# Kernel tuning notes

Hardware: AMD Instinct MI355X
Metric: run time of the kernel (lower is better)

The kernel has to match this reference:

```python
import jax, jax.numpy as jnp
import numpy as np

D = 256; H = 8; DK = D // H
NT, NW, ND = 2000, 50000, 20000
E_TT, E_WT, E_TD, E_WD = 128000, 256000, 320000, 320000
SQRT_DK = float(np.sqrt(DK))


def setup_inputs() -> dict:
    key = jax.random.key(0)
    ks = jax.random.split(key, 32)
    def nrm(i, shape, s=0.05):
        return jax.random.normal(ks[i], shape, jnp.float32) * s
    inp = {
        "feat_topic": nrm(0, (NT, D), 1.0),
        "feat_word": nrm(1, (NW, D), 1.0),
        "feat_doc": nrm(2, (ND, D), 1.0),
        "ht_prev": nrm(3, (NT, D), 1.0),
        # stacked per-ntype linears, index: 0=topic, 1=word, 2=doc
        "Wk": nrm(4, (3, D, D)), "bk": nrm(5, (3, D)),
        "Wq": nrm(6, (3, D, D)), "bq": nrm(7, (3, D)),
        "Wv": nrm(8, (3, D, D)), "bv": nrm(9, (3, D)),
        # a_linears, index: 0=topic, 1=doc
        "Wa": nrm(10, (2, D, D)), "ba": nrm(11, (2, D)),
        "ln_g": jnp.ones((2, D), jnp.float32),
        "ln_b": jnp.zeros((2, D), jnp.float32),
        "skip": jnp.ones((2,), jnp.float32),
        # RNNCell for topic
        "Wih": nrm(12, (D, D)), "Whh": nrm(13, (D, D)),
        "bih": nrm(14, (D,)), "bhh": nrm(15, (D,)),
        # relation params, index: 0=tt, 1=wt, 2=td, 3=wd
        "rel_pri": jnp.ones((4, H), jnp.float32),
        "rel_att": nrm(16, (4, H, DK, DK), 0.1),
        "rel_msg": nrm(17, (4, H, DK, DK), 0.1),
        "src_tt": jax.random.randint(ks[18], (E_TT,), 0, NT),
        "dst_tt": jnp.arange(E_TT, dtype=jnp.int32) % NT,
        "src_wt": jax.random.randint(ks[19], (E_WT,), 0, NW),
        "dst_wt": jnp.arange(E_WT, dtype=jnp.int32) % NT,
        "src_td": jax.random.randint(ks[20], (E_TD,), 0, NT),
        "dst_td": jnp.arange(E_TD, dtype=jnp.int32) % ND,
        "src_wd": jax.random.randint(ks[21], (E_WD,), 0, NW),
        "dst_wd": jnp.arange(E_WD, dtype=jnp.int32) % ND,
    }
    return inp


def _proj(x, W, b):
    return (x @ W + b).reshape(-1, H, DK)


def _layernorm(x, g, b):
    mu = x.mean(-1, keepdims=True)
    var = ((x - mu) ** 2).mean(-1, keepdims=True)
    return (x - mu) * jax.lax.rsqrt(var + 1e-5) * g + b


def _rel_message(k, v, q, src, dst, pri, A_att, A_msg, n_dst):
    # k,v: [N_src,H,DK]; q: [N_dst,H,DK]; per-edge gather-compute-scatter
    key = jnp.einsum('ehd,hdo->eho', k[src], A_att)          # [E,H,DK]
    att = (q[dst] * key).sum(-1) * pri / SQRT_DK             # [E,H]
    val = jnp.einsum('ehd,hdo->eho', v[src], A_msg)          # [E,H,DK]
    m = jax.ops.segment_max(att, dst, num_segments=n_dst)
    e = jnp.exp(att - m[dst])
    s = jax.ops.segment_sum(e, dst, num_segments=n_dst)
    a = e / s[dst]                                           # edge softmax per dst
    t = jax.ops.segment_sum(a[..., None] * val, dst, num_segments=n_dst)
    return jax.nn.relu(t.reshape(n_dst, D))


def reference(feat_topic, feat_word, feat_doc, ht_prev, Wk, bk, Wq, bq, Wv, bv,
              Wa, ba, ln_g, ln_b, skip, Wih, Whh, bih, bhh,
              rel_pri, rel_att, rel_msg,
              src_tt, dst_tt, src_wt, dst_wt, src_td, dst_td, src_wd, dst_wd):
    # ---- phase 1: messages into topic nodes (etypes tt, wt) ----
    k_t = _proj(feat_topic, Wk[0], bk[0]); v_t = _proj(feat_topic, Wv[0], bv[0])
    k_w = _proj(feat_word,  Wk[1], bk[1]); v_w = _proj(feat_word,  Wv[1], bv[1])
    q_t = _proj(feat_topic, Wq[0], bq[0])
    t_tt = _rel_message(k_t, v_t, q_t, src_tt, dst_tt, rel_pri[0], rel_att[0], rel_msg[0], NT)
    t_wt = _rel_message(k_w, v_w, q_t, src_wt, dst_wt, rel_pri[1], rel_att[1], rel_msg[1], NT)
    t_topic = 0.5 * (t_tt + t_wt)                            # cross_reducer='mean'
    alpha = jax.nn.sigmoid(skip[0])
    trans = t_topic @ Wa[0] + ba[0]
    mix = trans * alpha + feat_topic * (1.0 - alpha)
    h = jnp.tanh(mix @ Wih + bih + ht_prev @ Whh + bhh)      # RNNCell
    topic_out = _layernorm(h, ln_g[0], ln_b[0])
    # ---- phase 2: messages into doc nodes (etypes td, wd), topic uses updated feats ----
    k_t2 = _proj(topic_out, Wk[0], bk[0]); v_t2 = _proj(topic_out, Wv[0], bv[0])
    q_d = _proj(feat_doc, Wq[2], bq[2])
    t_td = _rel_message(k_t2, v_t2, q_d, src_td, dst_td, rel_pri[2], rel_att[2], rel_msg[2], ND)
    t_wd = _rel_message(k_w, v_w, q_d, src_wd, dst_wd, rel_pri[3], rel_att[3], rel_msg[3], ND)
    t_doc = 0.5 * (t_td + t_wd)
    alpha2 = jax.nn.sigmoid(skip[1])
    trans2 = t_doc @ Wa[1] + ba[1]
    mix2 = trans2 * alpha2 + feat_doc * (1.0 - alpha2)
    doc_out = _layernorm(mix2, ln_g[1], ln_b[1])
    return topic_out, doc_out
```

## Files before the change

### kernel.cpp

```cpp
#include <hip/hip_runtime.h>
#include <hip/hip_bf16.h>
#include <hip/hip_fp8.h>

typedef __attribute__((ext_vector_type(8))) short bf16x8;
typedef __attribute__((ext_vector_type(4))) float f32x4;
typedef __attribute__((ext_vector_type(2))) float f32x2;

constexpr int NT = 2000, NW = 50000, ND = 20000;
constexpr float INV_SQRT_DK = 0.17677669529663687f;

__device__ inline float bfu(unsigned short u) {
    return __uint_as_float(((unsigned int)u) << 16);
}
__device__ inline float blo(unsigned int u) { return __uint_as_float(u << 16); }
__device__ inline float bhi(unsigned int u) { return __uint_as_float(u & 0xffff0000u); }
__device__ inline short f2bf(float x) {
    __hip_bfloat16 h = __float2bfloat16(x);
    short s; __builtin_memcpy(&s, &h, 2); return s;
}

__device__ inline void dec4(unsigned int w, float* o) {
#if __has_builtin(__builtin_amdgcn_cvt_pk_f32_fp8)
    f32x2 a = __builtin_amdgcn_cvt_pk_f32_fp8(w, false);
    f32x2 b = __builtin_amdgcn_cvt_pk_f32_fp8(w, true);
    o[0] = a[0]; o[1] = a[1]; o[2] = b[0]; o[3] = b[1];
#else
    __hip_fp8_e4m3 t0, t1, t2, t3;
    t0.__x = (__hip_fp8_storage_t)(w & 0xff);
    t1.__x = (__hip_fp8_storage_t)((w >> 8) & 0xff);
    t2.__x = (__hip_fp8_storage_t)((w >> 16) & 0xff);
    t3.__x = (__hip_fp8_storage_t)((w >> 24) & 0xff);
    o[0] = (float)t0; o[1] = (float)t1; o[2] = (float)t2; o[3] = (float)t3;
#endif
}
__device__ inline unsigned char f2fp8(float v) {
#if __has_builtin(__builtin_amdgcn_cvt_pk_fp8_f32)
    return (unsigned char)(__builtin_amdgcn_cvt_pk_fp8_f32(v, v, 0u, false) & 0xff);
#else
    __hip_fp8_e4m3 h(v); return (unsigned char)h.__x;
#endif
}

__device__ inline void cstore(float* p, float v) { *p = v; }
__device__ inline void cstore(short* p, float v) { *p = f2bf(v); }
__device__ inline void cstore(unsigned char* p, float v) { *p = f2fp8(v); }

__device__ inline void cstore4(float* p, float4 v) {
    *reinterpret_cast<float4*>(p) = v;
}
__device__ inline void cstore4(short* p, float4 v) {
    short4 s; s.x = f2bf(v.x); s.y = f2bf(v.y); s.z = f2bf(v.z); s.w = f2bf(v.w);
    *reinterpret_cast<short4*>(p) = s;
}
__device__ inline void cstore4(unsigned char* p, float4 v) {
#if __has_builtin(__builtin_amdgcn_cvt_pk_fp8_f32)
    unsigned int w = __builtin_amdgcn_cvt_pk_fp8_f32(v.x, v.y, 0u, false);
    w = __builtin_amdgcn_cvt_pk_fp8_f32(v.z, v.w, w, true);
    *reinterpret_cast<unsigned int*>(p) = w;
#else
    p[0] = f2fp8(v.x); p[1] = f2fp8(v.y); p[2] = f2fp8(v.z); p[3] = f2fp8(v.w);
#endif
}

__device__ inline void gload16(const short* g, short* l) {
    __builtin_amdgcn_global_load_lds(
        (const __attribute__((address_space(1))) void*)g,
        (__attribute__((address_space(3))) void*)l, 16, 0, 0);
}

__device__ inline float dot32f8(const unsigned char* __restrict__ kp, const float* __restrict__ qh) {
    const uint4 u = *reinterpret_cast<const uint4*>(kp);
    const uint4 v = *reinterpret_cast<const uint4*>(kp + 16);
    const unsigned int ws[8] = {u.x, u.y, u.z, u.w, v.x, v.y, v.z, v.w};
    float d = 0.f;
    #pragma unroll
    for (int c = 0; c < 8; ++c) {
        float f[4];
        dec4(ws[c], f);
        d += qh[c * 4 + 0] * f[0] + qh[c * 4 + 1] * f[1]
           + qh[c * 4 + 2] * f[2] + qh[c * 4 + 3] * f[3];
    }
    return d;
}

__global__ __launch_bounds__(256) void fold_kernel(
    const float* __restrict__ Wk, const float* __restrict__ bk,
    const float* __restrict__ Wv, const float* __restrict__ bv,
    const float* __restrict__ rel_att, const float* __restrict__ rel_msg,
    short* __restrict__ B_t1, short* __restrict__ B_w, short* __restrict__ B_t2,
    float* __restrict__ bias_t1, float* __restrict__ bias_w, float* __restrict__ bias_t2)
{
    const int f = blockIdx.x >> 3, chunk = blockIdx.x & 7;
    const int rel = f >> 1, isV = f & 1;
    const int ntype = (rel == 1 || rel == 3) ? 1 : 0;
    const float* Wsrc = (isV ? Wv : Wk) + ntype * 65536;
    const float* bsrc = (isV ? bv : bk) + ntype * 256;
    const float* A    = (isV ? rel_msg : rel_att) + rel * 8192;
    short* wdst; float* bdst;
    switch (f) {
        case 0: wdst = B_t1 + 65536;     bdst = bias_t1 + 256; break;
        case 1: wdst = B_t1 + 2 * 65536; bdst = bias_t1 + 512; break;
        case 2: wdst = B_w;              bdst = bias_w;        break;
        case 3: wdst = B_w + 65536;      bdst = bias_w + 256;  break;
        case 4: wdst = B_t2;             bdst = bias_t2;       break;
        case 5: wdst = B_t2 + 65536;     bdst = bias_t2 + 256; break;
        case 6: wdst = B_w + 2 * 65536;  bdst = bias_w + 512;  break;
        default: wdst = B_w + 3 * 65536; bdst = bias_w + 768;  break;
    }
    __shared__ float Wsh[32][256];
    const int tid = threadIdx.x;
    for (int i = 0; i < 32; ++i)
        Wsh[i][tid] = Wsrc[(chunk * 32 + i) * 256 + tid];
    __syncthreads();
    const int h = tid >> 5, o = tid & 31;
    float a[32];
    #pragma unroll
    for (int d = 0; d < 32; ++d) a[d] = A[h * 1024 + d * 32 + o];
    short tmp[32];
    #pragma unroll
    for (int r = 0; r < 32; ++r) {
        float s = 0.f;
        #pragma unroll
        for (int d = 0; d < 32; ++d) s = fmaf(Wsh[r][(h << 5) + d], a[d], s);
        tmp[r] = f2bf(s);
    }
    short* wp = wdst + tid * 256 + chunk * 32;
    #pragma unroll
    for (int r8 = 0; r8 < 4; ++r8) {
        bf16x8 v;
        #pragma unroll
        for (int t = 0; t < 8; ++t) v[t] = tmp[r8 * 8 + t];
        *reinterpret_cast<bf16x8*>(wp + r8 * 8) = v;
    }
    if (chunk == 0) {
        float s = 0.f;
        #pragma unroll
        for (int d = 0; d < 32; ++d) s = fmaf(bsrc[(h << 5) + d], a[d], s);
        bdst[tid] = s;
    }
}

struct TransP { const float* s[6]; short* d[6]; };
__global__ __launch_bounds__(256) void wtrans6(TransP p) {
    const int m = blockIdx.y, n = blockIdx.x, k = threadIdx.x;
    p.d[m][n * 256 + k] = f2bf(p.s[m][k * 256 + n]);
}

__global__ void copy_bias(const float* __restrict__ s, float* __restrict__ d) {
    d[threadIdx.x] = s[threadIdx.x];
}

template <typename OutT, int EPI, int NI>
__device__ inline void epilogue(
    f32x4 (&acc)[NI][4], const float* __restrict__ bias, OutT* __restrict__ C,
    int M, int ldc, const float* __restrict__ extra,
    const float* __restrict__ skipv, int skipIdx,
    int row0, int col0, int wm, int wn, int r, int kb)
{
    float alpha = 0.f;
    if (EPI == 1) alpha = 1.f / (1.f + __expf(-skipv[skipIdx]));
    float4 b4[4];
    #pragma unroll
    for (int j = 0; j < 4; ++j)
        b4[j] = *reinterpret_cast<const float4*>(&bias[col0 + wn * 64 + j * 16 + kb * 4]);
    #pragma unroll
    for (int i = 0; i < NI; ++i) {
        const int rrow = row0 + wm * 64 + i * 16 + r;
        if (rrow >= M) continue;
        #pragma unroll
        for (int j = 0; j < 4; ++j) {
            const int cb = col0 + wn * 64 + j * 16 + kb * 4;
            float4 v;
            v.x = acc[i][j][0] + b4[j].x;
            v.y = acc[i][j][1] + b4[j].y;
            v.z = acc[i][j][2] + b4[j].z;
            v.w = acc[i][j][3] + b4[j].w;
            if (EPI == 1) {
                const float4 e = *reinterpret_cast<const float4*>(&extra[rrow * 256 + cb]);
                v.x = alpha * v.x + (1.f - alpha) * e.x;
                v.y = alpha * v.y + (1.f - alpha) * e.y;
                v.z = alpha * v.z + (1.f - alpha) * e.z;
                v.w = alpha * v.w + (1.f - alpha) * e.w;
            }
            if (EPI == 2) {
                const float4 e = *reinterpret_cast<const float4*>(&extra[rrow * 256 + cb]);
                v.x = tanhf(v.x + e.x);
                v.y = tanhf(v.y + e.y);
                v.z = tanhf(v.z + e.z);
                v.w = tanhf(v.w + e.w);
            }
            cstore4(C + rrow * ldc + cb, v);
        }
    }
}

template <bool XF32, typename OutT, int EPI, bool SWZ>
__global__ __launch_bounds__(256) void gemm_lds(
    const void* __restrict__ Xv, const short* __restrict__ Wt,
    const float* __restrict__ bias, OutT* __restrict__ C,
    int M, int ldc, const float* __restrict__ extra,
    const float* __restrict__ skipv, int skipIdx)
{
    __shared__ short As[128 * 64];
    __shared__ short Bs[128 * 64];
    int bxi = blockIdx.x, byi = blockIdx.y;
    if constexpr (SWZ) {
        const int h = bxi + (int)gridDim.x * byi;
        const int i = h >> 3;
        byi = (h & 7) + 8 * (i >> 3);
        bxi = i & 7;
        if (byi * 128 >= M) return;
    }
    const int tid = threadIdx.x;
    const int wave = tid >> 6, lane = tid & 63;
    const int wm = wave >> 1, wn = wave & 1;
    const int r = lane & 15, kb = lane >> 4;
    const int col0 = bxi * 128;
    const int row0 = byi * 128;

    const int l8 = lane >> 3;
    const int c8 = lane & 7;
    const int swz8 = c8 ^ l8;
    f32x4 acc[4][4] = {};

    for (int k0 = 0; k0 < 256; k0 += 64) {
        if (k0) __syncthreads();
        if constexpr (XF32) {
            #pragma unroll
            for (int q = 0; q < 4; ++q) {
                const int rl = wave * 32 + q * 8 + l8;
                const int grow = min(row0 + rl, M - 1);
                const float* xp = (const float*)Xv + grow * 256 + k0 + c8 * 8;
                const float4 x0 = *reinterpret_cast<const float4*>(xp);
                const float4 x1 = *reinterpret_cast<const float4*>(xp + 4);
                bf16x8 v;
                v[0] = f2bf(x0.x); v[1] = f2bf(x0.y); v[2] = f2bf(x0.z); v[3] = f2bf(x0.w);
                v[4] = f2bf(x1.x); v[5] = f2bf(x1.y); v[6] = f2bf(x1.z); v[7] = f2bf(x1.w);
                *reinterpret_cast<bf16x8*>(As + rl * 64 + swz8 * 8) = v;
            }
        } else {
            #pragma unroll
            for (int q = 0; q < 4; ++q) {
                const int rl = wave * 32 + q * 8 + l8;
                const int grow = min(row0 + rl, M - 1);
                gload16((const short*)Xv + grow * 256 + k0 + swz8 * 8,
                        As + (wave * 32 + q * 8) * 64);
            }
        }
        #pragma unroll
        for (int q = 0; q < 4; ++q) {
            const int cl = wave * 32 + q * 8 + l8;
            gload16(Wt + (col0 + cl) * 256 + k0 + swz8 * 8,
                    Bs + (wave * 32 + q * 8) * 64);
        }
        __syncthreads();
        #pragma unroll
        for (int s = 0; s < 2; ++s) {
            const int csw = ((kb + 4 * s) ^ (r & 7)) * 8;
            bf16x8 af[4], bw[4];
            #pragma unroll
            for (int i = 0; i < 4; ++i) {
                af[i] = *reinterpret_cast<const bf16x8*>(As + (wm * 64 + i * 16 + r) * 64 + csw);
                bw[i] = *reinterpret_cast<const bf16x8*>(Bs + (wn * 64 + i * 16 + r) * 64 + csw);
            }
            #pragma unroll
            for (int i = 0; i < 4; ++i)
                #pragma unroll
                for (int j = 0; j < 4; ++j)
                    acc[i][j] = __builtin_amdgcn_mfma_f32_16x16x32_bf16(bw[j], af[i], acc[i][j], 0, 0, 0);
        }
    }
    epilogue<OutT, EPI, 4>(acc, bias, C, M, ldc, extra, skipv, skipIdx,
                           row0, col0, wm, wn, r, kb);
}

__global__ __launch_bounds__(256) void gemm_qkv(
    const float* __restrict__ X, const short* __restrict__ Wt,
    const float* __restrict__ bias, short* __restrict__ Qo,
    unsigned char* __restrict__ KVo, int M)
{
    __shared__ short As[128 * 64];
    __shared__ short Bs[128 * 64];
    const int bxi = blockIdx.x, byi = blockIdx.y;
    const int tid = threadIdx.x;
    const int wave = tid >> 6, lane = tid & 63;
    const int wm = wave >> 1, wn = wave & 1;
    const int r = lane & 15, kb = lane >> 4;
    const int col0 = bxi * 128;
    const int row0 = byi * 128;

    const int l8 = lane >> 3;
    const int c8 = lane & 7;
    const int swz8 = c8 ^ l8;
    f32x4 acc[4][4] = {};

    for (int k0 = 0; k0 < 256; k0 += 64) {
        if (k0) __syncthreads();
        #pragma unroll
        for (int q = 0; q < 4; ++q) {
            const int rl = wave * 32 + q * 8 + l8;
            const int grow = min(row0 + rl, M - 1);
            const float* xp = X + grow * 256 + k0 + c8 * 8;
            const float4 x0 = *reinterpret_cast<const float4*>(xp);
            const float4 x1 = *reinterpret_cast<const float4*>(xp + 4);
            bf16x8 v;
            v[0] = f2bf(x0.x); v[1] = f2bf(x0.y); v[2] = f2bf(x0.z); v[3] = f2bf(x0.w);
            v[4] = f2bf(x1.x); v[5] = f2bf(x1.y); v[6] = f2bf(x1.z); v[7] = f2bf(x1.w);
            *reinterpret_cast<bf16x8*>(As + rl * 64 + swz8 * 8) = v;
        }
        #pragma unroll
        for (int q = 0; q < 4; ++q) {
            const int cl = wave * 32 + q * 8 + l8;
            gload16(Wt + (col0 + cl) * 256 + k0 + swz8 * 8,
                    Bs + (wave * 32 + q * 8) * 64);
        }
        __syncthreads();
        #pragma unroll
        for (int s = 0; s < 2; ++s) {
            const int csw = ((kb + 4 * s) ^ (r & 7)) * 8;
            bf16x8 af[4], bw[4];
            #pragma unroll
            for (int i = 0; i < 4; ++i) {
                af[i] = *reinterpret_cast<const bf16x8*>(As + (wm * 64 + i * 16 + r) * 64 + csw);
                bw[i] = *reinterpret_cast<const bf16x8*>(Bs + (wn * 64 + i * 16 + r) * 64 + csw);
            }
            #pragma unroll
            for (int i = 0; i < 4; ++i)
                #pragma unroll
                for (int j = 0; j < 4; ++j)
                    acc[i][j] = __builtin_amdgcn_mfma_f32_16x16x32_bf16(bw[j], af[i], acc[i][j], 0, 0, 0);
        }
    }

    float4 b4[4];
    #pragma unroll
    for (int j = 0; j < 4; ++j)
        b4[j] = *reinterpret_cast<const float4*>(&bias[col0 + wn * 64 + j * 16 + kb * 4]);
    #pragma unroll
    for (int i = 0; i < 4; ++i) {
        const int rrow = row0 + wm * 64 + i * 16 + r;
        if (rrow >= M) continue;
        #pragma unroll
        for (int j = 0; j < 4; ++j) {
            const int cb = col0 + wn * 64 + j * 16 + kb * 4;
            float4 v;
            v.x = acc[i][j][0] + b4[j].x;
            v.y = acc[i][j][1] + b4[j].y;
            v.z = acc[i][j][2] + b4[j].z;
            v.w = acc[i][j][3] + b4[j].w;
            if (bxi < 2) cstore4(Qo + rrow * 256 + cb, v);
            else         cstore4(KVo + rrow * 512 + (cb - 256), v);
        }
    }
}

template <bool XF32, typename OutT, int EPI, bool SWZ, bool SWAP>
__global__ __launch_bounds__(512) void gemm_w(
    const void* __restrict__ Xv, const short* __restrict__ Wt,
    const float* __restrict__ bias, OutT* __restrict__ C,
    int M, int ldc, const float* __restrict__ extra,
    const float* __restrict__ skipv, int skipIdx)
{
    __shared__ short As[256 * 64];
    __shared__ short Bs[128 * 64];
    int bxi = blockIdx.x, byi = blockIdx.y;
    if constexpr (SWZ) {
        const int h = bxi + (int)gridDim.x * byi;
        const int i = h >> 3;
        byi = (h & 7) + 8 * (i >> 3);
        bxi = i & 7;
        if (byi * 256 >= M) return;
    }
    const int tid = threadIdx.x;
    const int wave = tid >> 6, lane = tid & 63;
    const int wm = wave >> 1, wn = wave & 1;
    const int r = lane & 15, kb = lane >> 4;
    const int col0 = bxi * 128;
    const int row0 = byi * 256;

    const int l8 = lane >> 3;
    const int c8 = lane & 7;
    const int swz8 = c8 ^ l8;
    f32x4 acc[4][4] = {};

    for (int k0 = 0; k0 < 256; k0 += 64) {
        if (k0) __syncthreads();
        if constexpr (XF32) {
            #pragma unroll
            for (int q = 0; q < 4; ++q) {
                const int rl = wave * 32 + q * 8 + l8;
                const int grow = min(row0 + rl, M - 1);
                const float* xp = (const float*)Xv + grow * 256 + k0 + c8 * 8;
                const float4 x0 = *reinterpret_cast<const float4*>(xp);
                const float4 x1 = *reinterpret_cast<const float4*>(xp + 4);
                bf16x8 v;
                v[0] = f2bf(x0.x); v[1] = f2bf(x0.y); v[2] = f2bf(x0.z); v[3] = f2bf(x0.w);
                v[4] = f2bf(x1.x); v[5] = f2bf(x1.y); v[6] = f2bf(x1.z); v[7] = f2bf(x1.w);
                *reinterpret_cast<bf16x8*>(As + rl * 64 + swz8 * 8) = v;
            }
        } else {
            #pragma unroll
            for (int q = 0; q < 4; ++q) {
                const int rl = wave * 32 + q * 8 + l8;
                const int grow = min(row0 + rl, M - 1);
                gload16((const short*)Xv + grow * 256 + k0 + swz8 * 8,
                        As + (wave * 32 + q * 8) * 64);
            }
        }
        #pragma unroll
        for (int q = 0; q < 2; ++q) {
            const int cl = wave * 16 + q * 8 + l8;
            gload16(Wt + (col0 + cl) * 256 + k0 + swz8 * 8,
                    Bs + (wave * 16 + q * 8) * 64);
        }
        __syncthreads();
        #pragma unroll
        for (int s = 0; s < 2; ++s) {
            const int csw = ((kb + 4 * s) ^ (r & 7)) * 8;
            bf16x8 af[4], bw[4];
            #pragma unroll
            for (int i = 0; i < 4; ++i) {
                af[i] = *reinterpret_cast<const bf16x8*>(As + (wm * 64 + i * 16 + r) * 64 + csw);
                bw[i] = *reinterpret_cast<const bf16x8*>(Bs + (wn * 64 + i * 16 + r) * 64 + csw);
            }
            #pragma unroll
            for (int i = 0; i < 4; ++i)
                #pragma unroll
                for (int j = 0; j < 4; ++j) {
                    if constexpr (SWAP)
                        acc[i][j] = __builtin_amdgcn_mfma_f32_16x16x32_bf16(bw[j], af[i], acc[i][j], 0, 0, 0);
                    else
                        acc[i][j] = __builtin_amdgcn_mfma_f32_16x16x32_bf16(af[i], bw[j], acc[i][j], 0, 0, 0);
                }
        }
    }

    if constexpr (SWAP) {
        epilogue<OutT, EPI, 4>(acc, bias, C, M, ldc, extra, skipv, skipIdx,
                               row0, col0, wm, wn, r, kb);
    } else {
        float alpha = 0.f;
        if (EPI == 1) alpha = 1.f / (1.f + __expf(-skipv[skipIdx]));
        #pragma unroll
        for (int i = 0; i < 4; ++i) {
            #pragma unroll
            for (int j = 0; j < 4; ++j) {
                const int col = col0 + wn * 64 + j * 16 + r;
                const float bc = bias[col];
                #pragma unroll
                for (int t = 0; t < 4; ++t) {
                    const int rrow = row0 + wm * 64 + i * 16 + kb * 4 + t;
                    if (rrow < M) {
                        float v = acc[i][j][t] + bc;
                        if (EPI == 1) v = alpha * v + (1.f - alpha) * extra[rrow * 256 + col];
                        if (EPI == 2) v = tanhf(v + extra[rrow * 256 + col]);
                        cstore(C + rrow * ldc + col, v);
                    }
                }
            }
        }
    }
}

template <int NE>
__device__ inline void rel_scores_f8(const unsigned char* __restrict__ kv, int ld, int koff,
                                     const int* __restrict__ sidx, int off, float scale,
                                     const float* __restrict__ qh, float* __restrict__ sc,
                                     int g, int l)
{
    constexpr int NL = NE / 32;
    float att[NL];
    #pragma unroll
    for (int t = 0; t < NL; ++t)
        att[t] = dot32f8(kv + (size_t)sidx[off + l + 32 * t] * ld + koff + g * 32, qh) * scale;
    float m = att[0];
    #pragma unroll
    for (int t = 1; t < NL; ++t) m = fmaxf(m, att[t]);
    #pragma unroll
    for (int o = 16; o > 0; o >>= 1) m = fmaxf(m, __shfl_xor(m, o));
    float ex[NL], s = 0.f;
    #pragma unroll
    for (int t = 0; t < NL; ++t) { ex[t] = __expf(att[t] - m); s += ex[t]; }
    #pragma unroll
    for (int o = 16; o > 0; o >>= 1) s += __shfl_xor(s, o);
    const float inv = 1.f / s;
    #pragma unroll
    for (int t = 0; t < NL; ++t) sc[(off + l + 32 * t) * 9 + g] = ex[t] * inv;
}

template <int NE>
__device__ inline void accum_f8(const unsigned char* __restrict__ kv, int ld, int voff,
                                const int* __restrict__ sidx, int off,
                                const float* __restrict__ sc,
                                int es, int ct, int h, float* __restrict__ acc)
{
    #pragma unroll
    for (int e = es; e < NE; e += 8) {
        const float w = sc[(off + e) * 9 + h];
        const uint2 u = *reinterpret_cast<const uint2*>(
            kv + (size_t)sidx[off + e] * ld + voff + ct * 8);
        float f[8];
        dec4(u.x, f); dec4(u.y, f + 4);
        #pragma unroll
        for (int k = 0; k < 8; ++k) acc[k] = fmaf(w, f[k], acc[k]);
    }
}

template <int NEA, int NEB>
__global__ __launch_bounds__(256) void msg_k(
    const short* __restrict__ q, int ldq,
    const unsigned char* __restrict__ kvA, int ldA, int koffA, int voffA,
    const int* __restrict__ srcA,
    const unsigned char* __restrict__ kvB, int ldB, int koffB, int voffB,
    const int* __restrict__ srcB,
    const float* __restrict__ relPri, int relA, int relB,
    short* __restrict__ out, int n_dst)
{
    constexpr int NET = NEA + NEB;
    const int j = blockIdx.x, tid = threadIdx.x;
    __shared__ float qsh[256];
    __shared__ int sidx[NET];
    __shared__ float sc[NET * 9];
    __shared__ float psA[8][256];
    __shared__ float psB[8][256];

    qsh[tid] = bfu((unsigned short)q[j * ldq + tid]);
    if (tid < NEA) sidx[tid] = srcA[j + tid * n_dst];
    else if (tid < NET) sidx[tid] = srcB[j + (tid - NEA) * n_dst];
    __syncthreads();

    const int g = tid >> 5, l = tid & 31;
    float qr[32];
    #pragma unroll
    for (int c = 0; c < 8; ++c) {
        const float4 v = *reinterpret_cast<const float4*>(qsh + g * 32 + c * 4);
        qr[c * 4] = v.x; qr[c * 4 + 1] = v.y; qr[c * 4 + 2] = v.z; qr[c * 4 + 3] = v.w;
    }

    if constexpr (NEA == 16 && NEB == 16) {
        const int isB = l >> 4;
        const unsigned char* base = isB ? kvB + koffB : kvA + koffA;
        const int ld = isB ? ldB : ldA;
        const float scale = relPri[(isB ? relB : relA) * 8 + g] * INV_SQRT_DK;
        const float att = dot32f8(base + (size_t)sidx[l] * ld + g * 32, qr) * scale;
        float m = att;
        #pragma unroll
        for (int o = 8; o > 0; o >>= 1) m = fmaxf(m, __shfl_xor(m, o));
        const float ex = __expf(att - m);
        float s = ex;
        #pragma unroll
        for (int o = 8; o > 0; o >>= 1) s += __shfl_xor(s, o);
        sc[l * 9 + g] = ex / s;
    } else {
        rel_scores_f8<NEA>(kvA, ldA, koffA, sidx, 0,
                           relPri[relA * 8 + g] * INV_SQRT_DK, qr, sc, g, l);
        rel_scores_f8<NEB>(kvB, ldB, koffB, sidx, NEA,
                           relPri[relB * 8 + g] * INV_SQRT_DK, qr, sc, g, l);
    }
    __syncthreads();

    const int es = tid >> 5, ct = tid & 31, hh = ct >> 2;
    float accA[8] = {}, accB[8] = {};
    accum_f8<NEA>(kvA, ldA, voffA, sidx, 0,   sc, es, ct, hh, accA);
    accum_f8<NEB>(kvB, ldB, voffB, sidx, NEA, sc, es, ct, hh, accB);
    const int sw = ct & 4;
    *reinterpret_cast<float4*>(&psA[es][(ct * 8) ^ sw])     = make_float4(accA[0], accA[1], accA[2], accA[3]);
    *reinterpret_cast<float4*>(&psA[es][(ct * 8 + 4) ^ sw]) = make_float4(accA[4], accA[5], accA[6], accA[7]);
    *reinterpret_cast<float4*>(&psB[es][(ct * 8) ^ sw])     = make_float4(accB[0], accB[1], accB[2], accB[3]);
    *reinterpret_cast<float4*>(&psB[es][(ct * 8 + 4) ^ sw]) = make_float4(accB[4], accB[5], accB[6], accB[7]);
    __syncthreads();

    float rA = 0.f, rB = 0.f;
    const int rp = tid ^ ((tid >> 3) & 4);
    #pragma unroll
    for (int e2 = 0; e2 < 8; ++e2) { rA += psA[e2][rp]; rB += psB[e2][rp]; }
    out[j * 256 + tid] = f2bf(0.5f * (fmaxf(rA, 0.f) + fmaxf(rB, 0.f)));
}

template <bool WB>
__global__ __launch_bounds__(256) void ln_k(
    float* __restrict__ data, const float* __restrict__ g,
    const float* __restrict__ b, int nrows, short* __restrict__ bfout)
{
    const int wid = threadIdx.x >> 6, lane = threadIdx.x & 63;
    const int row = blockIdx.x * 4 + wid;
    if (row >= nrows) return;
    float4 x = *reinterpret_cast<float4*>(data + row * 256 + lane * 4);
    float s  = x.x + x.y + x.z + x.w;
    float q2 = x.x * x.x + x.y * x.y + x.z * x.z + x.w * x.w;
    #pragma unroll
    for (int o = 32; o > 0; o >>= 1) { s += __shfl_xor(s, o); q2 += __shfl_xor(q2, o); }
    const float mu  = s * (1.f / 256.f);
    const float var = q2 * (1.f / 256.f) - mu * mu;
    const float rr = rsqrtf(var + 1e-5f);
    const float4 gg = *reinterpret_cast<const float4*>(g + lane * 4);
    const float4 bb = *reinterpret_cast<const float4*>(b + lane * 4);
    x.x = (x.x - mu) * rr * gg.x + bb.x;
    x.y = (x.y - mu) * rr * gg.y + bb.y;
    x.z = (x.z - mu) * rr * gg.z + bb.z;
    x.w = (x.w - mu) * rr * gg.w + bb.w;
    *reinterpret_cast<float4*>(data + row * 256 + lane * 4) = x;
    if (WB) {
        ushort4 u;
        u.x = (unsigned short)f2bf(x.x); u.y = (unsigned short)f2bf(x.y);
        u.z = (unsigned short)f2bf(x.z); u.w = (unsigned short)f2bf(x.w);
        *reinterpret_cast<ushort4*>((unsigned short*)bfout + row * 256 + lane * 4) = u;
    }
}

extern "C" void kernel_launch(void* const* d_in, const int* in_sizes, int n_in,
                              void* d_out, int out_size, void* d_ws, size_t ws_size,
                              hipStream_t stream)
{
    const float* feat_topic = (const float*)d_in[0];
    const float* feat_word  = (const float*)d_in[1];
    const float* feat_doc   = (const float*)d_in[2];
    const float* ht_prev    = (const float*)d_in[3];
    const float* Wk  = (const float*)d_in[4];
    const float* bk  = (const float*)d_in[5];
    const float* Wq  = (const float*)d_in[6];
    const float* bq  = (const float*)d_in[7];
    const float* Wv  = (const float*)d_in[8];
    const float* bv  = (const float*)d_in[9];
    const float* Wa  = (const float*)d_in[10];
    const float* ba  = (const float*)d_in[11];
    const float* ln_g = (const float*)d_in[12];
    const float* ln_b = (const float*)d_in[13];
    const float* skip = (const float*)d_in[14];
    const float* Wih  = (const float*)d_in[15];
    const float* Whh  = (const float*)d_in[16];
    const float* bih  = (const float*)d_in[17];
    const float* bhh  = (const float*)d_in[18];
    const float* rel_pri = (const float*)d_in[19];
    const float* rel_att = (const float*)d_in[20];
    const float* rel_msg = (const float*)d_in[21];
    const int* src_tt = (const int*)d_in[22];
    const int* src_wt = (const int*)d_in[24];
    const int* src_td = (const int*)d_in[26];
    const int* src_wd = (const int*)d_in[28];

    short* B_t1 = (short*)d_ws;
    short* B_w  = B_t1 + 196608;
    short* B_t2 = B_w + 262144;
    short* Wq2t = B_t2 + 131072;
    short* Whht = Wq2t + 65536;
    short* Wa0t = Whht + 65536;
    short* Wiht = Wa0t + 65536;
    short* Wa1t = Wiht + 65536;
    short* q_t  = Wa1t + 65536;
    unsigned char* kv1 = (unsigned char*)(q_t + 512000);
    unsigned char* w8  = kv1 + 1024000;
    unsigned char* kv2 = w8 + 51200000;
    short* qd   = (short*)(kv2 + 1024000);
    short* ttop = qd + 5120000;
    short* mixb = ttop + 512000;
    short* tdoc = mixb + 512000;
    short* xt2  = tdoc + 5120000;
    float* bias_t1 = (float*)(xt2 + 512000);
    float* bias_w  = bias_t1 + 768;
    float* bias_t2 = bias_w + 1024;
    float* r2      = bias_t2 + 512;

    float* out_topic = (float*)d_out;
    float* out_doc   = out_topic + NT * 256;

    fold_kernel<<<dim3(64), 256, 0, stream>>>(Wk, bk, Wv, bv, rel_att, rel_msg,
                                              B_t1, B_w, B_t2, bias_t1, bias_w, bias_t2);
    TransP tp;
    tp.s[0] = Wq;            tp.d[0] = B_t1;
    tp.s[1] = Wq + 131072;   tp.d[1] = Wq2t;
    tp.s[2] = Whh;           tp.d[2] = Whht;
    tp.s[3] = Wih;           tp.d[3] = Wiht;
    tp.s[4] = Wa;            tp.d[4] = Wa0t;
    tp.s[5] = Wa + 65536;    tp.d[5] = Wa1t;
    wtrans6<<<dim3(256, 6), 256, 0, stream>>>(tp);
    copy_bias<<<dim3(1), 256, 0, stream>>>(bq, bias_t1);

    gemm_w<true, unsigned char, 0, true, false><<<dim3(8, 200), 512, 0, stream>>>(
        feat_word, B_w, bias_w, w8, NW, 1024, nullptr, nullptr, 0);

    gemm_qkv<<<dim3(6, 16), 256, 0, stream>>>(
        feat_topic, B_t1, bias_t1, q_t, kv1, NT);
    gemm_w<true, short, 0, false, true><<<dim3(2, 79), 512, 0, stream>>>(
        feat_doc, Wq2t, bq + 512, qd, ND, 256, nullptr, nullptr, 0);
    gemm_lds<true, float, 0, false><<<dim3(2, 16), 256, 0, stream>>>(
        ht_prev, Whht, bhh, r2, NT, 256, nullptr, nullptr, 0);

    msg_k<64, 128><<<dim3(NT), 256, 0, stream>>>(
        q_t, 256,
        kv1, 512, 0, 256, src_tt,
        w8, 1024, 0, 256, src_wt,
        rel_pri, 0, 1, ttop, NT);

    gemm_lds<false, short, 1, false><<<dim3(2, 16), 256, 0, stream>>>(
        ttop, Wa0t, ba, mixb, NT, 256, feat_topic, skip, 0);
    gemm_lds<false, float, 2, false><<<dim3(2, 16), 256, 0, stream>>>(
        mixb, Wiht, bih, out_topic, NT, 256, r2, nullptr, 0);
    ln_k<true><<<dim3(500), 256, 0, stream>>>(out_topic, ln_g, ln_b, NT, xt2);

    gemm_lds<false, unsigned char, 0, false><<<dim3(4, 16), 256, 0, stream>>>(
        xt2, B_t2, bias_t2, kv2, NT, 512, nullptr, nullptr, 0);

    msg_k<16, 16><<<dim3(ND), 256, 0, stream>>>(
        qd, 256,
        kv2, 512, 0, 256, src_td,
        w8, 1024, 512, 768, src_wd,
        rel_pri, 2, 3, tdoc, ND);

    gemm_w<false, float, 1, false, true><<<dim3(2, 79), 512, 0, stream>>>(
        tdoc, Wa1t, ba + 256, out_doc, ND, 256, feat_doc, skip, 1);
    ln_k<false><<<dim3(5000), 256, 0, stream>>>(out_doc, ln_g + 256, ln_b + 256, ND, nullptr);
}
```

Baseline: 254.0 us.

## Split value accumulation across relations with 16-byte fp8 loads and vectorized output

In the message kernel, the value-accumulation phase now gives each half-warp one relation (A or B). Each thread loads 16 fp8 values (uint4) instead of 8 for both relations, which halves the per-thread gather count and merges the two partial-sum buffers into one padded shared array. The q load and the bf16 output store are also vectorized, with the output staged through shared memory for 16-byte writes. The cost is an extra barrier and a 16-float accumulator per thread, which may raise register pressure.

Result: no change. 254.7 us (+0.3%).

```diff
diff --git a/kernel.cpp b/kernel.cpp
--- a/kernel.cpp
+++ b/kernel.cpp
@@ -488,24 +488,6 @@
     for (int t = 0; t < NL; ++t) sc[(off + l + 32 * t) * 9 + g] = ex[t] * inv;
 }
 
-template <int NE>
-__device__ inline void accum_f8(const unsigned char* __restrict__ kv, int ld, int voff,
-                                const int* __restrict__ sidx, int off,
-                                const float* __restrict__ sc,
-                                int es, int ct, int h, float* __restrict__ acc)
-{
-    #pragma unroll
-    for (int e = es; e < NE; e += 8) {
-        const float w = sc[(off + e) * 9 + h];
-        const uint2 u = *reinterpret_cast<const uint2*>(
-            kv + (size_t)sidx[off + e] * ld + voff + ct * 8);
-        float f[8];
-        dec4(u.x, f); dec4(u.y, f + 4);
-        #pragma unroll
-        for (int k = 0; k < 8; ++k) acc[k] = fmaf(w, f[k], acc[k]);
-    }
-}
-
 template <int NEA, int NEB>
 __global__ __launch_bounds__(256) void msg_k(
     const short* __restrict__ q, int ldq,
@@ -521,10 +503,14 @@
     __shared__ float qsh[256];
     __shared__ int sidx[NET];
     __shared__ float sc[NET * 9];
-    __shared__ float psA[8][256];
-    __shared__ float psB[8][256];
-
-    qsh[tid] = bfu((unsigned short)q[j * ldq + tid]);
+    __shared__ float ps[8][544];
+
+    if (tid < 64) {
+        const ushort4 u = *reinterpret_cast<const ushort4*>(
+            (const unsigned short*)q + j * ldq + tid * 4);
+        float4 f; f.x = bfu(u.x); f.y = bfu(u.y); f.z = bfu(u.z); f.w = bfu(u.w);
+        *reinterpret_cast<float4*>(qsh + tid * 4) = f;
+    }
     if (tid < NEA) sidx[tid] = srcA[j + tid * n_dst];
     else if (tid < NET) sidx[tid] = srcB[j + (tid - NEA) * n_dst];
     __syncthreads();
@@ -559,22 +545,44 @@
     }
     __syncthreads();
 
-    const int es = tid >> 5, ct = tid & 31, hh = ct >> 2;
-    float accA[8] = {}, accB[8] = {};
-    accum_f8<NEA>(kvA, ldA, voffA, sidx, 0,   sc, es, ct, hh, accA);
-    accum_f8<NEB>(kvB, ldB, voffB, sidx, NEA, sc, es, ct, hh, accB);
-    const int sw = ct & 4;
-    *reinterpret_cast<float4*>(&psA[es][(ct * 8) ^ sw])     = make_float4(accA[0], accA[1], accA[2], accA[3]);
-    *reinterpret_cast<float4*>(&psA[es][(ct * 8 + 4) ^ sw]) = make_float4(accA[4], accA[5], accA[6], accA[7]);
-    *reinterpret_cast<float4*>(&psB[es][(ct * 8) ^ sw])     = make_float4(accB[0], accB[1], accB[2], accB[3]);
-    *reinterpret_cast<float4*>(&psB[es][(ct * 8 + 4) ^ sw]) = make_float4(accB[4], accB[5], accB[6], accB[7]);
+    const int ct16 = tid & 15;
+    const int rel  = (tid >> 4) & 1;
+    const int es   = tid >> 5;
+    const int hh   = ct16 >> 1;
+    const unsigned char* kvR = rel ? kvB : kvA;
+    const int ldR   = rel ? ldB : ldA;
+    const int voffR = rel ? voffB : voffA;
+    const int offR  = rel ? NEA : 0;
+    const int neR   = rel ? NEB : NEA;
+    float acc[16] = {};
+    for (int e = es; e < neR; e += 8) {
+        const float w = sc[(offR + e) * 9 + hh];
+        const uint4 u = *reinterpret_cast<const uint4*>(
+            kvR + (size_t)sidx[offR + e] * ldR + voffR + ct16 * 16);
+        float f[16];
+        dec4(u.x, f); dec4(u.y, f + 4); dec4(u.z, f + 8); dec4(u.w, f + 12);
+        #pragma unroll
+        for (int k = 0; k < 16; ++k) acc[k] = fmaf(w, f[k], acc[k]);
+    }
+    {
+        float* pp = &ps[es][rel * 272 + ct16 * 17];
+        #pragma unroll
+        for (int k = 0; k < 16; ++k) pp[k] = acc[k];
+    }
     __syncthreads();
 
+    const int ra = (tid >> 4) * 17 + (tid & 15);
     float rA = 0.f, rB = 0.f;
-    const int rp = tid ^ ((tid >> 3) & 4);
-    #pragma unroll
-    for (int e2 = 0; e2 < 8; ++e2) { rA += psA[e2][rp]; rB += psB[e2][rp]; }
-    out[j * 256 + tid] = f2bf(0.5f * (fmaxf(rA, 0.f) + fmaxf(rB, 0.f)));
+    #pragma unroll
+    for (int e2 = 0; e2 < 8; ++e2) { rA += ps[e2][ra]; rB += ps[e2][272 + ra]; }
+    const float val = 0.5f * (fmaxf(rA, 0.f) + fmaxf(rB, 0.f));
+    unsigned short* ob = (unsigned short*)qsh;
+    ob[tid] = (unsigned short)f2bf(val);
+    __syncthreads();
+    if (tid < 32) {
+        const uint4 u = *reinterpret_cast<const uint4*>(ob + tid * 8);
+        *reinterpret_cast<uint4*>((unsigned short*)out + j * 256 + tid * 8) = u;
+    }
 }
 
 template <bool WB>
```
